# Performance work log

Measured on AMD Instinct MI355X. Metric: run time of the kernel, lower is better.

## Reference

```python
import jax, jax.numpy as jnp
import numpy as np

N, E, G = 50000, 150000, 200
D, ED_IN, EH = 320, 15, 32
NB, NT = 3, 9  # conv blocks, edge types


def setup_inputs() -> dict:
    key = jax.random.key(0)
    ks = jax.random.split(key, 16)
    s = 0.02
    return {
        "x": jax.random.normal(ks[0], (N, D), jnp.float32),
        "batch": jnp.sort(jax.random.randint(ks[1], (N,), 0, G)),
        "edge_indices": jax.random.randint(ks[2], (NT, 2, E), 0, N),
        "edge_attrs": jax.random.normal(ks[3], (NT, E, ED_IN), jnp.float32),
        "W1": jax.random.normal(ks[4], (2 * D + ED_IN, EH), jnp.float32) * s,
        "b1": jnp.zeros((EH,), jnp.float32),
        "W2": jax.random.normal(ks[5], (EH, EH), jnp.float32) * s,
        "b2": jnp.zeros((EH,), jnp.float32),
        "Wq": jax.random.normal(ks[6], (NB, NT, D, D), jnp.float32) * s,
        "bq": jnp.zeros((NB, NT, D), jnp.float32),
        "Wk": jax.random.normal(ks[7], (NB, NT, D, D), jnp.float32) * s,
        "bk": jnp.zeros((NB, NT, D), jnp.float32),
        "Wv": jax.random.normal(ks[8], (NB, NT, D, D), jnp.float32) * s,
        "bv": jnp.zeros((NB, NT, D), jnp.float32),
        "We": jax.random.normal(ks[9], (NB, NT, EH, D), jnp.float32) * s,
        "be": jnp.zeros((NB, NT, D), jnp.float32),
        "Ws": jax.random.normal(ks[10], (NB, NT, D, D), jnp.float32) * s,
        "bs": jnp.zeros((NB, NT, D), jnp.float32),
        "gamma": jnp.ones((NB, D), jnp.float32),
        "beta": jnp.zeros((NB, D), jnp.float32),
    }


def _transformer_conv(x, src, dst, ea, Wq, bq, Wk, bk, Wv, bv, We, be, Ws, bs):
    # PyG TransformerConv, heads=1, edge_dim=EH, eval mode (no dropout).
    q = (x @ Wq + bq)[dst]                    # [E, D] query at destination
    e = ea @ We + be                          # [E, D] projected edge attr
    k = (x @ Wk + bk)[src] + e                # [E, D]
    v = (x @ Wv + bv)[src] + e                # [E, D]
    alpha = (q * k).sum(-1) / jnp.sqrt(jnp.float32(D))  # [E]
    amax = jax.ops.segment_max(alpha, dst, num_segments=N)
    amax = jnp.where(jnp.isfinite(amax), amax, 0.0)     # guard empty segments
    ex = jnp.exp(alpha - amax[dst])
    denom = jax.ops.segment_sum(ex, dst, num_segments=N)
    w = ex / (denom[dst] + 1e-16)
    out = jax.ops.segment_sum(w[:, None] * v, dst, num_segments=N)
    return out + x @ Ws + bs                  # root/skip connection


def _graph_layer_norm(x, batch, gamma, beta):
    # PyG gnn.norm.LayerNorm, mode='graph': normalize per graph over nodes+channels.
    cnt = jax.ops.segment_sum(jnp.ones((N,), x.dtype), batch, num_segments=G)
    norm = jnp.maximum(cnt, 1.0) * D          # elements per graph
    mean = jax.ops.segment_sum(x.sum(-1), batch, num_segments=G) / norm
    xc = x - mean[batch][:, None]
    var = jax.ops.segment_sum((xc * xc).sum(-1), batch, num_segments=G) / norm
    out = xc / jnp.sqrt(var + 1e-5)[batch][:, None]
    return out * gamma + beta


def reference(x, batch, edge_indices, edge_attrs, W1, b1, W2, b2,
              Wq, bq, Wk, bk, Wv, bv, We, be, Ws, bs, gamma, beta):
    # Edge MLP preprocessing (uses original node features x).
    new_ea = []
    for t in range(NT):
        src, dst = edge_indices[t, 0], edge_indices[t, 1]
        cat = jnp.concatenate([x[src], x[dst], edge_attrs[t]], axis=-1)  # [E, 655]
        h = jax.nn.leaky_relu(cat @ W1 + b1)
        new_ea.append(h @ W2 + b2)

    h = x
    for b in range(NB):
        acc = jnp.zeros_like(h)
        for t in range(NT):
            src, dst = edge_indices[t, 0], edge_indices[t, 1]
            acc = acc + _transformer_conv(
                h, src, dst, new_ea[t],
                Wq[b, t], bq[b, t], Wk[b, t], bk[b, t], Wv[b, t], bv[b, t],
                We[b, t], be[b, t], Ws[b, t], bs[b, t])
        x_ = jax.nn.leaky_relu(acc / 9.0)
        x_ = _graph_layer_norm(x_, batch, gamma[b], beta[b])
        h = 0.5 * (h + x_)

    return jax.ops.segment_max(h, batch, num_segments=G)  # global max pool [G, D]
```

## Files before the change

kernel.cpp:

```cpp
#include <hip/hip_runtime.h>

#define N_NODES 50000
#define N_EDGE  150000
#define N_GRAPH 200
#define DIM     320
#define EDI     15
#define EH      32
#define NBLK    3
#define NTYP    9
#define NPAD    51200
#define BPT     50
#define QLD     676
#define QCOLS   673
#define NPQ     768

typedef unsigned short u16;
typedef unsigned int   u32;
typedef __bf16 bf16x8 __attribute__((ext_vector_type(8)));
typedef float  f32x4  __attribute__((ext_vector_type(4)));

__device__ __forceinline__ float b2f(u16 s) {
    u32 u = ((u32)s) << 16;
    return __builtin_bit_cast(float, u);
}
__device__ __forceinline__ float b2f_lo(u32 u) { return __builtin_bit_cast(float, u << 16); }
__device__ __forceinline__ float b2f_hi(u32 u) { return __builtin_bit_cast(float, u & 0xffff0000u); }
__device__ __forceinline__ u16 f2b(float f) {
    u32 u = __builtin_bit_cast(u32, f);
    u = (u + 0x7fffu + ((u >> 16) & 1u)) >> 16;
    return (u16)u;
}

__device__ __forceinline__ void gll16(const u16* g, u32 ldsAddr) {
    u32 m0v = (u32)__builtin_amdgcn_readfirstlane((int)ldsAddr);
    asm volatile("s_mov_b32 m0, %0\n\t"
                 "global_load_lds_dwordx4 %1, off"
                 :: "s"(m0v), "v"((unsigned long long)(size_t)g)
                 : "memory");
}

__global__ __launch_bounds__(256) void gemm_kernel(
    const u16* __restrict__ A, int Mstride,
    const u16* __restrict__ Bst, const float* __restrict__ bias,
    u16* __restrict__ Cb, float* __restrict__ Cf,
    int ldc, int out_cols, int M, int NP, int KQ, int mode)
{
    const int tid = threadIdx.x;
    const int wave = tid >> 6, lane = tid & 63;

    const int nwg = gridDim.x * gridDim.y;
    const int flat = blockIdx.y * gridDim.x + blockIdx.x;
    const int qq = nwg >> 3, rr = nwg & 7;
    const int xcd = flat & 7, loc = flat >> 3;
    const int swz = (xcd < rr ? xcd * (qq + 1) : rr * (qq + 1) + (xcd - rr) * qq) + loc;
    const int n0 = (swz % gridDim.x) * 128, m0 = (swz / gridDim.x) * 128;

    const int wm = (wave & 1) << 6, wn = (wave >> 1) << 6;
    const int lm = lane & 15, quad = lane >> 4;

    __shared__ uint4 smem[2][2][512];
    const u32 ldsBase = (u32)(size_t)&smem[0][0][0];

    f32x4 acc[4][4] = {};
    const int nIter = KQ >> 2;

    auto stage = [&](int s, int buf) {
        const int c0 = s << 2;
        const u32 bufBase = ldsBase + (u32)buf * 16384u;
#pragma unroll
        for (int u = 0; u < 2; ++u) {
            const int i = wave + (u << 2);
            const int chunk = i >> 1, half = (i & 1) << 6;
            const u16* ga = A + ((size_t)(c0 + chunk) * Mstride + m0 + half + lane) * 8;
            gll16(ga, bufBase + (u32)i * 1024u);
            const u16* gb = Bst + ((size_t)(c0 + chunk) * NP + n0 + half + lane) * 8;
            gll16(gb, bufBase + 8192u + (u32)i * 1024u);
        }
    };

    stage(0, 0);
    asm volatile("s_waitcnt vmcnt(0)" ::: "memory");
    __syncthreads();

    int cur = 0;
    for (int s = 0; s < nIter; ++s) {
        if (s + 1 < nIter) stage(s + 1, cur ^ 1);
        const uint4* aT = &smem[cur][0][0];
        const uint4* bT = &smem[cur][1][0];
        bf16x8 af[4], bfr[4];
#pragma unroll
        for (int mi = 0; mi < 4; ++mi)
            af[mi] = __builtin_bit_cast(bf16x8, aT[quad * 128 + wm + mi * 16 + lm]);
#pragma unroll
        for (int ni = 0; ni < 4; ++ni)
            bfr[ni] = __builtin_bit_cast(bf16x8, bT[quad * 128 + wn + ni * 16 + lm]);
#pragma unroll
        for (int mi = 0; mi < 4; ++mi)
#pragma unroll
            for (int ni = 0; ni < 4; ++ni)
                acc[mi][ni] = __builtin_amdgcn_mfma_f32_16x16x32_bf16(af[mi], bfr[ni], acc[mi][ni], 0, 0, 0);
        asm volatile("s_waitcnt vmcnt(0)" ::: "memory");
        __syncthreads();
        cur ^= 1;
    }

#pragma unroll
    for (int mi = 0; mi < 4; ++mi) {
        int row = m0 + wm + mi * 16 + quad * 4;
#pragma unroll
        for (int ni = 0; ni < 4; ++ni) {
            int col = n0 + wn + ni * 16 + lm;
            float bv = bias ? bias[col] : 0.f;
#pragma unroll
            for (int r = 0; r < 4; ++r) {
                int rr2 = row + r;
                if (rr2 < M && col < out_cols) {
                    float v = acc[mi][ni][r] + bv;
                    size_t off = (size_t)rr2 * ldc + col;
                    if (mode == 0)      Cb[off] = f2b(v);
                    else if (mode == 1) Cf[off] = v;
                    else                Cf[off] += v;
                }
            }
        }
    }
}

__global__ void k_convert_x(const float* __restrict__ x, u16* __restrict__ hb,
                            u16* __restrict__ hNode) {
    int i = blockIdx.x * 256 + threadIdx.x;
    if (i >= N_NODES * DIM) return;
    int node = i / DIM, c = i - node * DIM;
    u16 v = f2b(x[i]);
    hb[((size_t)(c >> 3) * N_NODES + node) * 8 + (c & 7)] = v;
    hNode[i] = v;
}

__global__ __launch_bounds__(256) void k_prep_M(
    const float* __restrict__ Wq, const float* __restrict__ Wk,
    float* __restrict__ Mf)
{
    __shared__ float aq[16][321];
    __shared__ float ak[16][321];
    int bt = blockIdx.z, e0 = blockIdx.y * 16, d0 = blockIdx.x * 16;
    const float* wq = Wq + ((size_t)bt * 320 + e0) * 320;
    const float* wk = Wk + ((size_t)bt * 320 + d0) * 320;
    for (int i = threadIdx.x; i < 16 * 320; i += 256) {
        int r = i / 320, j = i - r * 320;
        aq[r][j] = wq[(size_t)r * 320 + j];
        ak[r][j] = wk[(size_t)r * 320 + j];
    }
    __syncthreads();
    int te = threadIdx.x >> 4, td = threadIdx.x & 15;
    float s = 0.f;
    for (int j = 0; j < 320; ++j) s += aq[te][j] * ak[td][j];
    Mf[((size_t)bt * 320 + e0 + te) * 320 + d0 + td] = s;
}

__global__ void k_prep_qkvW(const float* __restrict__ Mf, const float* __restrict__ Wv,
                            u16* __restrict__ Bst) {
    int i = blockIdx.x * 256 + threadIdx.x;
    if (i >= 27 * 40 * NPQ) return;
    int col = i % NPQ, kq = (i / NPQ) % 40, bt = i / (NPQ * 40);
    if (col >= 640 && col < QCOLS) return;
    u16 tmp[8];
    if (col >= QCOLS) {
#pragma unroll
        for (int r = 0; r < 8; ++r) tmp[r] = 0;
    } else if (col < 320) {
#pragma unroll
        for (int r = 0; r < 8; ++r)
            tmp[r] = f2b(Mf[((size_t)bt * 320 + kq * 8 + r) * 320 + col]);
    } else {
#pragma unroll
        for (int r = 0; r < 8; ++r)
            tmp[r] = f2b(Wv[((size_t)bt * 320 + kq * 8 + r) * 320 + (col - 320)]);
    }
    *(uint4*)(&Bst[(((size_t)bt * 40 + kq) * NPQ + col) * 8]) = *(uint4*)tmp;
}

__global__ __launch_bounds__(256) void k_prep_ext(
    const float* __restrict__ Wq, const float* __restrict__ bq,
    const float* __restrict__ We, const float* __restrict__ be,
    const float* __restrict__ bk,
    u16* __restrict__ Bst, float* __restrict__ biasQkv)
{
    __shared__ float WeL[33 * 321];
    int bt = blockIdx.x, kt = blockIdx.y;
    for (int i = threadIdx.x; i < 33 * 320; i += 256) {
        int r = i / 320, d = i - r * 320;
        WeL[r * 321 + d] = (r < 32) ? We[((size_t)bt * 32 + r) * 320 + d]
                                    : (be[(size_t)bt * 320 + d] + bk[(size_t)bt * 320 + d]);
    }
    __syncthreads();
    if (kt < 10) {
        int k  = kt * 32 + (threadIdx.x >> 3);
        int ct = threadIdx.x & 7;
        const float* wq = Wq + ((size_t)bt * 320 + k) * 320;
        float dot[5] = {0.f, 0.f, 0.f, 0.f, 0.f};
        for (int d = 0; d < 320; ++d) {
            float w = wq[d];
            dot[0] += w * WeL[ct * 321 + d];
            dot[1] += w * WeL[(ct + 8) * 321 + d];
            dot[2] += w * WeL[(ct + 16) * 321 + d];
            dot[3] += w * WeL[(ct + 24) * 321 + d];
            dot[4] += w * WeL[32 * 321 + d];
        }
#pragma unroll
        for (int u = 0; u < 4; ++u)
            Bst[(((size_t)bt * 40 + (k >> 3)) * NPQ + 640 + ct + u * 8) * 8 + (k & 7)] = f2b(dot[u]);
        if (ct == 0)
            Bst[(((size_t)bt * 40 + (k >> 3)) * NPQ + 672) * 8 + (k & 7)] = f2b(dot[4]);
    } else {
        int c = threadIdx.x;
        if (c < 33) {
            const float* b = bq + (size_t)bt * 320;
            float s = 0.f;
            for (int d = 0; d < 320; ++d) s += b[d] * WeL[c * 321 + d];
            biasQkv[bt * 1024 + 640 + c] = s;
        }
    }
}

__global__ __launch_bounds__(256) void k_prep_qkvB(
    const float* __restrict__ Wk, const float* __restrict__ bq,
    const float* __restrict__ bv, float* __restrict__ bias)
{
    int i = blockIdx.x * 256 + threadIdx.x;
    if (i >= 27 * NPQ) return;
    int col = i % NPQ, bt = i / NPQ;
    if (col < 320) {
        const float4* wr = (const float4*)(Wk + ((size_t)bt * 320 + col) * 320);
        const float4* bb = (const float4*)(bq + (size_t)bt * 320);
        float s = 0.f;
        for (int j = 0; j < 80; ++j) {
            float4 a = wr[j], b = bb[j];
            s += a.x * b.x + a.y * b.y + a.z * b.z + a.w * b.w;
        }
        bias[bt * 1024 + col] = s;
    } else if (col < 640) {
        bias[bt * 1024 + col] = bv[(size_t)bt * 320 + (col - 320)];
    } else if (col >= QCOLS) {
        bias[bt * 1024 + col] = 0.f;
    }
}

__global__ void k_prep_skipW(const float* __restrict__ Ws, u16* __restrict__ Bst) {
    int i = blockIdx.x * 256 + threadIdx.x;
    if (i >= 3 * 320 * 384) return;
    int col = i % 384, k = (i / 384) % 320, b = i / (384 * 320);
    float v = 0.f;
    if (col < 320)
        for (int t = 0; t < 9; ++t)
            v += Ws[((size_t)(b * 9 + t) * 320 + k) * 320 + col];
    Bst[(((size_t)b * 40 + (k >> 3)) * 384 + col) * 8 + (k & 7)] = f2b(v);
}
__global__ void k_prep_skipB(const float* __restrict__ bs, float* __restrict__ bias) {
    int i = blockIdx.x * 256 + threadIdx.x;
    if (i >= 3 * 384) return;
    int col = i % 384, b = i / 384;
    float v = 0.f;
    if (col < 320)
        for (int t = 0; t < 9; ++t) v += bs[(b * 9 + t) * 320 + col];
    bias[i] = v;
}

__global__ void k_prep_sWe(const float* __restrict__ We, const float* __restrict__ be,
                           u16* __restrict__ Bst) {
    int i = blockIdx.x * 256 + threadIdx.x;
    if (i >= 3 * 40 * 384) return;
    int col = i % 384, kq = (i / 384) % 40, b = i / (384 * 40);
    u16 tmp[8];
#pragma unroll
    for (int r = 0; r < 8; ++r) {
        int k = kq * 8 + r;
        float v = 0.f;
        if (col < 320 && k < 306) {
            int t = k / 34, j = k - t * 34;
            int bt = b * 9 + t;
            if (j < 32)       v = We[((size_t)bt * 32 + j) * 320 + col];
            else if (j == 32) v = be[(size_t)bt * 320 + col];
        }
        tmp[r] = f2b(v);
    }
    *(uint4*)(&Bst[(((size_t)b * 40 + kq) * 384 + col) * 8]) = *(uint4*)tmp;
}

__global__ void k_prep_w1W(const float* __restrict__ W1, u16* __restrict__ Bst) {
    int i = blockIdx.x * 256 + threadIdx.x;
    if (i >= 320 * 128) return;
    int col = i & 127, k = i >> 7;
    float v = 0.f;
    if (col < 32)      v = W1[(size_t)k * 32 + col];
    else if (col < 64) v = W1[(size_t)(320 + k) * 32 + (col - 32)];
    Bst[((size_t)(k >> 3) * 128 + col) * 8 + (k & 7)] = f2b(v);
}

__global__ void k_csr_zero(int* __restrict__ cnt) {
    int i = blockIdx.x * 256 + threadIdx.x;
    if (i < NTYP * NPAD) cnt[i] = 0;
}
__global__ void k_csr_count(const int* __restrict__ eidx, int* __restrict__ cnt) {
    int i = blockIdx.x * 256 + threadIdx.x;
    if (i >= NTYP * N_EDGE) return;
    int t = i / N_EDGE, e = i - t * N_EDGE;
    int dst = eidx[(size_t)(t * 2 + 1) * N_EDGE + e];
    atomicAdd(&cnt[t * NPAD + dst], 1);
}
__global__ __launch_bounds__(1024) void k_csr_scan1(const int* __restrict__ cnt,
                                                    int* __restrict__ rowStart,
                                                    int* __restrict__ blockSum) {
    __shared__ int tmp[1024];
    int t = blockIdx.y, blk = blockIdx.x, tid = threadIdx.x;
    int idx = t * NPAD + blk * 1024 + tid;
    int v = cnt[idx];
    tmp[tid] = v;
    __syncthreads();
    for (int off = 1; off < 1024; off <<= 1) {
        int x = (tid >= off) ? tmp[tid - off] : 0;
        __syncthreads();
        tmp[tid] += x;
        __syncthreads();
    }
    rowStart[idx] = tmp[tid] - v;
    if (tid == 1023) blockSum[t * 64 + blk] = tmp[tid];
}
__global__ void k_csr_scan2(int* __restrict__ blockSum) {
    int t = threadIdx.x;
    if (t >= NTYP) return;
    int run = 0;
    for (int b = 0; b < BPT; ++b) {
        int v = blockSum[t * 64 + b];
        blockSum[t * 64 + b] = run;
        run += v;
    }
}
__global__ void k_csr_scan3(int* __restrict__ rowStart, const int* __restrict__ blockSum,
                            int* __restrict__ cursor) {
    int i = blockIdx.x * 256 + threadIdx.x;
    if (i >= NTYP * NPAD) return;
    int t = i / NPAD, n = i - t * NPAD;
    int v = rowStart[i] + blockSum[t * 64 + (n >> 10)];
    rowStart[i] = v;
    cursor[i] = v;
}
__global__ void k_csr_scatter(const int* __restrict__ eidx, int* __restrict__ cursor,
                              u16* __restrict__ sSrc, int* __restrict__ sEid) {
    int i = blockIdx.x * 256 + threadIdx.x;
    if (i >= NTYP * N_EDGE) return;
    int t = i / N_EDGE, e = i - t * N_EDGE;
    int src = eidx[(size_t)(t * 2) * N_EDGE + e];
    int dst = eidx[(size_t)(t * 2 + 1) * N_EDGE + e];
    int pos = atomicAdd(&cursor[t * NPAD + dst], 1);
    sSrc[(size_t)t * N_EDGE + pos] = (u16)src;
    sEid[(size_t)t * N_EDGE + pos] = e;
}

__global__ __launch_bounds__(256) void k_edge_mlp(
    const u16* __restrict__ Anodes, const int* __restrict__ eidx,
    const float* __restrict__ eattr, const float* __restrict__ W1,
    const float* __restrict__ b1, const float* __restrict__ W2,
    const float* __restrict__ b2, u16* __restrict__ outEa, int t)
{
    __shared__ float w1c[EDI][EH];
    __shared__ float w2s[EH][EH];
    __shared__ float b1s[EH], b2s[EH];
    int tid = threadIdx.x;
    for (int i = tid; i < EDI * EH; i += 256) w1c[i / EH][i % EH] = W1[(640 + i / EH) * EH + (i % EH)];
    for (int i = tid; i < EH * EH; i += 256) w2s[i / EH][i % EH] = W2[i];
    if (tid < EH) { b1s[tid] = b1[tid]; b2s[tid] = b2[tid]; }
    __syncthreads();

    int e = blockIdx.x * 256 + tid;
    if (e >= N_EDGE) return;
    int src = eidx[(size_t)(t * 2) * N_EDGE + e];
    int dst = eidx[(size_t)(t * 2 + 1) * N_EDGE + e];
    const float* eat = eattr + ((size_t)t * N_EDGE + e) * EDI;
    const u16* a1 = Anodes + (size_t)src * 64;
    const u16* a2 = Anodes + (size_t)dst * 64 + 32;

    float h1[EH];
#pragma unroll
    for (int j = 0; j < EH; ++j) h1[j] = b2f(a1[j]) + b2f(a2[j]) + b1s[j];
    for (int i = 0; i < EDI; ++i) {
        float v = eat[i];
#pragma unroll
        for (int j = 0; j < EH; ++j) h1[j] += v * w1c[i][j];
    }
#pragma unroll
    for (int j = 0; j < EH; ++j) h1[j] = h1[j] > 0.f ? h1[j] : 0.01f * h1[j];

    u16* orow = outEa + (size_t)e * EH;
    for (int j = 0; j < EH; ++j) {
        float o = b2s[j];
#pragma unroll
        for (int i = 0; i < EH; ++i) o += h1[i] * w2s[i][j];
        orow[j] = f2b(o);
    }
}

__global__ __launch_bounds__(256) void k_attn(
    const u16* __restrict__ qkv, const u16* __restrict__ hNode,
    const int* __restrict__ rowStart,
    const u16* __restrict__ sSrc, const int* __restrict__ sEid,
    const u16* __restrict__ ea, float* __restrict__ acc,
    u16* __restrict__ sST, int t34)
{
    int wave = threadIdx.x >> 6, lane = threadIdx.x & 63;
    int n = blockIdx.x * 4 + wave;
    if (n >= N_NODES) return;
    int eb = rowStart[n], ee = rowStart[n + 1];
    if (eb == ee) return;

    const u16* qrow = qkv + (size_t)n * QLD;
    uint2 qv = *(const uint2*)(qrow + 4 * lane);
    float q40 = b2f_lo(qv.x), q41 = b2f_hi(qv.x);
    float q42 = b2f_lo(qv.y), q43 = b2f_hi(qv.y);
    float q1 = b2f(qrow[256 + lane]);
    float qwl = (lane < 33) ? b2f(qrow[640 + lane]) : 0.f;
    float qwbe = __shfl(qwl, 32, 64);
    float qw = (lane < 32) ? qwl : 0.f;
    const float RS = 0.05590169943749474f;

    float m = -INFINITY, l = 0.f, as = 0.f;
    float av0 = 0.f, av1 = 0.f, av2 = 0.f, av3 = 0.f, avt = 0.f;

    int ei = eb;
    for (; ei + 2 <= ee; ei += 2) {
        int s0 = sSrc[ei], s1 = sSrc[ei + 1];
        int id0 = sEid[ei], id1 = sEid[ei + 1];
        const u16* kr0 = hNode + (size_t)s0 * DIM;
        const u16* kr1 = hNode + (size_t)s1 * DIM;
        uint2 k0v = *(const uint2*)(kr0 + 4 * lane);
        uint2 k1v = *(const uint2*)(kr1 + 4 * lane);
        float k0t = b2f(kr0[256 + lane]);
        float k1t = b2f(kr1[256 + lane]);
        float ea0 = (lane < 32) ? b2f(ea[(size_t)id0 * 32 + lane]) : 0.f;
        float ea1 = (lane < 32) ? b2f(ea[(size_t)id1 * 32 + lane]) : 0.f;
        float d0 = qw * ea0 + q1 * k0t
                 + q40 * b2f_lo(k0v.x) + q41 * b2f_hi(k0v.x)
                 + q42 * b2f_lo(k0v.y) + q43 * b2f_hi(k0v.y);
        float d1 = qw * ea1 + q1 * k1t
                 + q40 * b2f_lo(k1v.x) + q41 * b2f_hi(k1v.x)
                 + q42 * b2f_lo(k1v.y) + q43 * b2f_hi(k1v.y);
#pragma unroll
        for (int off = 32; off > 0; off >>= 1) {
            d0 += __shfl_xor(d0, off, 64);
            d1 += __shfl_xor(d1, off, 64);
        }
        float a0 = (d0 + qwbe) * RS, a1 = (d1 + qwbe) * RS;
        float mn = fmaxf(m, fmaxf(a0, a1));
        float sc = __expf(m - mn);
        float p0 = __expf(a0 - mn), p1 = __expf(a1 - mn);
        l = l * sc + p0 + p1;
        const u16* vr0 = qkv + (size_t)s0 * QLD + 320;
        const u16* vr1 = qkv + (size_t)s1 * QLD + 320;
        uint2 v0v = *(const uint2*)(vr0 + 4 * lane);
        uint2 v1v = *(const uint2*)(vr1 + 4 * lane);
        float v0t = b2f(vr0[256 + lane]), v1t = b2f(vr1[256 + lane]);
        av0 = av0 * sc + p0 * b2f_lo(v0v.x) + p1 * b2f_lo(v1v.x);
        av1 = av1 * sc + p0 * b2f_hi(v0v.x) + p1 * b2f_hi(v1v.x);
        av2 = av2 * sc + p0 * b2f_lo(v0v.y) + p1 * b2f_lo(v1v.y);
        av3 = av3 * sc + p0 * b2f_hi(v0v.y) + p1 * b2f_hi(v1v.y);
        avt = avt * sc + p0 * v0t + p1 * v1t;
        as = as * sc + p0 * ea0 + p1 * ea1;
        m = mn;
    }
    if (ei < ee) {
        int s0 = sSrc[ei];
        int id0 = sEid[ei];
        const u16* kr0 = hNode + (size_t)s0 * DIM;
        uint2 k0v = *(const uint2*)(kr0 + 4 * lane);
        float k0t = b2f(kr0[256 + lane]);
        float ea0 = (lane < 32) ? b2f(ea[(size_t)id0 * 32 + lane]) : 0.f;
        float d0 = qw * ea0 + q1 * k0t
                 + q40 * b2f_lo(k0v.x) + q41 * b2f_hi(k0v.x)
                 + q42 * b2f_lo(k0v.y) + q43 * b2f_hi(k0v.y);
#pragma unroll
        for (int off = 32; off > 0; off >>= 1) d0 += __shfl_xor(d0, off, 64);
        float a0 = (d0 + qwbe) * RS;
        float mn = fmaxf(m, a0);
        float sc = __expf(m - mn), p0 = __expf(a0 - mn);
        l = l * sc + p0;
        const u16* vr0 = qkv + (size_t)s0 * QLD + 320;
        uint2 v0v = *(const uint2*)(vr0 + 4 * lane);
        float v0t = b2f(vr0[256 + lane]);
        av0 = av0 * sc + p0 * b2f_lo(v0v.x);
        av1 = av1 * sc + p0 * b2f_hi(v0v.x);
        av2 = av2 * sc + p0 * b2f_lo(v0v.y);
        av3 = av3 * sc + p0 * b2f_hi(v0v.y);
        avt = avt * sc + p0 * v0t;
        as = as * sc + p0 * ea0;
    }

    float inv = 1.f / l;
    float* arow = acc + (size_t)n * DIM;
    f32x4 pa = *(const f32x4*)(arow + 4 * lane);
    pa[0] += av0 * inv; pa[1] += av1 * inv;
    pa[2] += av2 * inv; pa[3] += av3 * inv;
    *(f32x4*)(arow + 4 * lane) = pa;
    arow[256 + lane] += avt * inv;
    if (lane < 33) {
        int k = t34 + lane;
        float sv = (lane < 32) ? as * inv : 1.f;
        sST[((size_t)(k >> 3) * N_NODES + n) * 8 + (k & 7)] = f2b(sv);
    }
}

__device__ __forceinline__ int lowerb(const int* a, int n, int v) {
    int lo = 0, hi = n;
    while (lo < hi) { int mid = (lo + hi) >> 1; if (a[mid] < v) lo = mid + 1; else hi = mid; }
    return lo;
}

__global__ __launch_bounds__(1024) void k_post(
    const float* __restrict__ acc, u16* __restrict__ hb, u16* __restrict__ hNode,
    const int* __restrict__ batch, const float* __restrict__ gamma,
    const float* __restrict__ beta)
{
    int g = blockIdx.x;
    int start = lowerb(batch, N_NODES, g);
    int end   = lowerb(batch, N_NODES, g + 1);
    int cnt = end - start;
    if (cnt == 0) return;
    int i0 = start * DIM, i1 = end * DIM;

    float s = 0.f, ss = 0.f;
    for (int i = i0 + threadIdx.x; i < i1; i += 1024) {
        float v = acc[i] * (1.f / 9.f);
        v = v > 0.f ? v : 0.01f * v;
        s += v; ss += v * v;
    }
    __shared__ float rs[16], rss[16];
#pragma unroll
    for (int off = 32; off > 0; off >>= 1) { s += __shfl_xor(s, off, 64); ss += __shfl_xor(ss, off, 64); }
    int wave = threadIdx.x >> 6, lane = threadIdx.x & 63;
    if (lane == 0) { rs[wave] = s; rss[wave] = ss; }
    __syncthreads();
    if (threadIdx.x == 0) {
        float S = 0.f, SS = 0.f;
        for (int w = 0; w < 16; ++w) { S += rs[w]; SS += rss[w]; }
        float norm = (float)cnt * DIM;
        float mean = S / norm;
        float var = SS / norm - mean * mean;
        rs[0] = mean;
        rss[0] = rsqrtf(var + 1e-5f);
    }
    __syncthreads();
    float mean = rs[0], rsig = rss[0];
    for (int i = i0 + threadIdx.x; i < i1; i += 1024) {
        float v = acc[i] * (1.f / 9.f);
        v = v > 0.f ? v : 0.01f * v;
        int node = i / DIM, c = i - node * DIM;
        float o = (v - mean) * rsig * gamma[c] + beta[c];
        u16 nb = f2b(0.5f * (b2f(hNode[i]) + o));
        hNode[i] = nb;
        hb[((size_t)(c >> 3) * N_NODES + node) * 8 + (c & 7)] = nb;
    }
}

__global__ __launch_bounds__(320) void k_maxpool(
    const u16* __restrict__ hb, const int* __restrict__ batch, float* __restrict__ out)
{
    int g = blockIdx.x, c = threadIdx.x;
    int start = lowerb(batch, N_NODES, g);
    int end   = lowerb(batch, N_NODES, g + 1);
    size_t base = (size_t)(c >> 3) * N_NODES * 8 + (c & 7);
    float m = -INFINITY;
    for (int n = start; n < end; ++n) m = fmaxf(m, b2f(hb[base + (size_t)n * 8]));
    out[(size_t)g * DIM + c] = m;
}

extern "C" void kernel_launch(void* const* d_in, const int* in_sizes, int n_in,
                              void* d_out, int out_size, void* d_ws, size_t ws_size,
                              hipStream_t stream)
{
    (void)in_sizes; (void)n_in; (void)out_size;
    const float* x     = (const float*)d_in[0];
    const int*   batch = (const int*)d_in[1];
    const int*   eidx  = (const int*)d_in[2];
    const float* eattr = (const float*)d_in[3];
    const float* W1 = (const float*)d_in[4];
    const float* b1 = (const float*)d_in[5];
    const float* W2 = (const float*)d_in[6];
    const float* b2 = (const float*)d_in[7];
    const float* Wq = (const float*)d_in[8];
    const float* bq = (const float*)d_in[9];
    const float* Wk = (const float*)d_in[10];
    const float* bk = (const float*)d_in[11];
    const float* Wv = (const float*)d_in[12];
    const float* bv = (const float*)d_in[13];
    const float* We = (const float*)d_in[14];
    const float* be = (const float*)d_in[15];
    const float* Ws = (const float*)d_in[16];
    const float* bs = (const float*)d_in[17];
    const float* gamma = (const float*)d_in[18];
    const float* beta  = (const float*)d_in[19];
    float* out = (float*)d_out;

    char* base = (char*)d_ws;
    size_t off = 0;
    auto carve = [&](size_t bytes) -> char* {
        char* r = base + off;
        off += (bytes + 255) & ~(size_t)255;
        return r;
    };
    u16*   hbKq    = (u16*)  carve((size_t)40 * N_NODES * 8 * 2 + 1024);
    u16*   hNode   = (u16*)  carve((size_t)N_NODES * DIM * 2);
    float* acc     = (float*)carve((size_t)N_NODES * DIM * 4);
    u16*   qkv     = (u16*)  carve((size_t)N_NODES * QLD * 2);
    u16*   sST     = (u16*)  carve((size_t)40 * N_NODES * 8 * 2 + 1024);
    u16*   Anodes  = (u16*)  carve((size_t)N_NODES * 64 * 2);
    float* Mf      = (float*)carve((size_t)27 * 320 * 320 * 4);
    u16*   BstQkv  = (u16*)  carve((size_t)27 * 40 * NPQ * 8 * 2);
    float* biasQkv = (float*)carve((size_t)27 * 1024 * 4);
    u16*   BstSkip = (u16*)  carve((size_t)3 * 40 * 384 * 8 * 2);
    float* biasSkip= (float*)carve((size_t)3 * 384 * 4);
    u16*   BstSWe  = (u16*)  carve((size_t)3 * 40 * 384 * 8 * 2);
    u16*   BstW1   = (u16*)  carve((size_t)40 * 128 * 8 * 2);
    int*   cnt     = (int*)  carve((size_t)NTYP * NPAD * 4);
    int*   rowStart= (int*)  carve((size_t)NTYP * NPAD * 4);
    int*   blockSum= (int*)  carve((size_t)NTYP * 64 * 4);
    u16*   sSrc    = (u16*)  carve((size_t)NTYP * N_EDGE * 2);
    int*   sEid    = (int*)  carve((size_t)NTYP * N_EDGE * 4);
    size_t fixed = off;
    size_t bigBytes   = (size_t)NTYP * N_EDGE * EH * 2;
    size_t smallBytes = (size_t)N_EDGE * EH * 2;
    int bigEa = (ws_size >= fixed + bigBytes + (1u << 20)) ? 1 : 0;
    u16* newEa = (u16*)carve(bigEa ? bigBytes : smallBytes);

    k_convert_x<<<(N_NODES * DIM + 255) / 256, 256, 0, stream>>>(x, hbKq, hNode);
    k_prep_M<<<dim3(20, 20, 27), 256, 0, stream>>>(Wq, Wk, Mf);
    k_prep_qkvW<<<(27 * 40 * NPQ + 255) / 256, 256, 0, stream>>>(Mf, Wv, BstQkv);
    k_prep_ext<<<dim3(27, 11), 256, 0, stream>>>(Wq, bq, We, be, bk, BstQkv, biasQkv);
    k_prep_qkvB<<<(27 * NPQ + 255) / 256, 256, 0, stream>>>(Wk, bq, bv, biasQkv);
    k_prep_skipW<<<(3 * 320 * 384 + 255) / 256, 256, 0, stream>>>(Ws, BstSkip);
    k_prep_skipB<<<(3 * 384 + 255) / 256, 256, 0, stream>>>(bs, biasSkip);
    k_prep_sWe<<<(3 * 40 * 384 + 255) / 256, 256, 0, stream>>>(We, be, BstSWe);
    k_prep_w1W<<<(320 * 128 + 255) / 256, 256, 0, stream>>>(W1, BstW1);

    k_csr_zero<<<(NTYP * NPAD + 255) / 256, 256, 0, stream>>>(cnt);
    k_csr_count<<<(NTYP * N_EDGE + 255) / 256, 256, 0, stream>>>(eidx, cnt);
    k_csr_scan1<<<dim3(BPT, NTYP), 1024, 0, stream>>>(cnt, rowStart, blockSum);
    k_csr_scan2<<<1, 64, 0, stream>>>(blockSum);
    k_csr_scan3<<<(NTYP * NPAD + 255) / 256, 256, 0, stream>>>(rowStart, blockSum, cnt);
    k_csr_scatter<<<(NTYP * N_EDGE + 255) / 256, 256, 0, stream>>>(eidx, cnt, sSrc, sEid);

    const int mt = (N_NODES + 127) / 128;
    const int et = (N_EDGE + 255) / 256;
    gemm_kernel<<<dim3(1, mt), 256, 0, stream>>>(hbKq, N_NODES, BstW1, nullptr,
                                                 Anodes, nullptr, 64, 64, N_NODES, 128, 40, 0);
    if (bigEa) {
        for (int t = 0; t < NTYP; ++t)
            k_edge_mlp<<<dim3(et), 256, 0, stream>>>(
                Anodes, eidx, eattr, W1, b1, W2, b2, newEa + (size_t)t * N_EDGE * EH, t);
    }

    for (int b = 0; b < NBLK; ++b) {
        gemm_kernel<<<dim3(3, mt), 256, 0, stream>>>(
            hbKq, N_NODES, BstSkip + (size_t)b * 40 * 384 * 8, biasSkip + b * 384,
            nullptr, acc, DIM, DIM, N_NODES, 384, 40, 1);
        hipMemsetAsync(sST, 0, (size_t)40 * N_NODES * 8 * 2, stream);
        for (int t = 0; t < NTYP; ++t) {
            int bt = b * NTYP + t;
            u16* eaT = bigEa ? (newEa + (size_t)t * N_EDGE * EH) : newEa;
            if (!bigEa)
                k_edge_mlp<<<dim3(et), 256, 0, stream>>>(
                    Anodes, eidx, eattr, W1, b1, W2, b2, eaT, t);
            gemm_kernel<<<dim3(6, mt), 256, 0, stream>>>(
                hbKq, N_NODES, BstQkv + (size_t)bt * 40 * NPQ * 8, biasQkv + bt * 1024,
                qkv, nullptr, QLD, QCOLS, N_NODES, NPQ, 40, 0);
            k_attn<<<dim3((N_NODES + 3) / 4), 256, 0, stream>>>(
                qkv, hNode, rowStart + t * NPAD, sSrc + (size_t)t * N_EDGE, sEid + (size_t)t * N_EDGE,
                eaT, acc, sST, t * 34);
        }
        gemm_kernel<<<dim3(3, mt), 256, 0, stream>>>(
            sST, N_NODES, BstSWe + (size_t)b * 40 * 384 * 8, nullptr,
            nullptr, acc, DIM, DIM, N_NODES, 384, 40, 2);
        k_post<<<N_GRAPH, 1024, 0, stream>>>(acc, hbKq, hNode, batch,
                                             gamma + b * DIM, beta + b * DIM);
    }
    k_maxpool<<<N_GRAPH, 320, 0, stream>>>(hbKq, batch, out);
}
```

Measured before the change: 5.768 ms.

## Defer V projection: aggregate raw source features, apply Wv in batched GEMMs

The per-type QKV GEMM no longer computes the V columns, which halves its output width. The attention kernel instead aggregates the softmax-weighted raw source node features and edge attributes into a bf16 K-major staging buffer. Wv, We, the biases and the skip weights are then applied through grouped GEMMs with larger K that accumulate into acc every two edge types. The Wq·Wk^T precompute also moves onto the MFMA GEMM with a batched z dimension. This trades per-type V GEMM work for fewer, deeper GEMMs and lighter attention writes, but adds bf16 rounding of the aggregated features and a more complex buffer-reuse layout.

After: 5.523 ms. 1.04x faster.

```diff
diff --git a/kernel.cpp b/kernel.cpp
--- a/kernel.cpp
+++ b/kernel.cpp
@@ -10,9 +10,11 @@
 #define NTYP    9
 #define NPAD    51200
 #define BPT     50
-#define QLD     676
-#define QCOLS   673
-#define NPQ     768
+#define QLD     360
+#define QCOLS   353
+#define NPQ     384
+#define HAGCH   132
+#define BIGCH   448
 
 typedef unsigned short u16;
 typedef unsigned int   u32;
@@ -43,8 +45,14 @@
     const u16* __restrict__ A, int Mstride,
     const u16* __restrict__ Bst, const float* __restrict__ bias,
     u16* __restrict__ Cb, float* __restrict__ Cf,
-    int ldc, int out_cols, int M, int NP, int KQ, int mode)
-{
+    int ldc, int out_cols, int M, int NP, int KQ, int mode,
+    int zA, int zB, int zC)
+{
+    A += (size_t)blockIdx.z * zA;
+    Bst += (size_t)blockIdx.z * zB;
+    if (Cb) Cb += (size_t)blockIdx.z * zC;
+    if (Cf) Cf += (size_t)blockIdx.z * zC;
+
     const int tid = threadIdx.x;
     const int wave = tid >> 6, lane = tid & 63;
 
@@ -136,45 +144,30 @@
     hNode[i] = v;
 }
 
-__global__ __launch_bounds__(256) void k_prep_M(
-    const float* __restrict__ Wq, const float* __restrict__ Wk,
-    float* __restrict__ Mf)
-{
-    __shared__ float aq[16][321];
-    __shared__ float ak[16][321];
-    int bt = blockIdx.z, e0 = blockIdx.y * 16, d0 = blockIdx.x * 16;
-    const float* wq = Wq + ((size_t)bt * 320 + e0) * 320;
-    const float* wk = Wk + ((size_t)bt * 320 + d0) * 320;
-    for (int i = threadIdx.x; i < 16 * 320; i += 256) {
-        int r = i / 320, j = i - r * 320;
-        aq[r][j] = wq[(size_t)r * 320 + j];
-        ak[r][j] = wk[(size_t)r * 320 + j];
-    }
-    __syncthreads();
-    int te = threadIdx.x >> 4, td = threadIdx.x & 15;
-    float s = 0.f;
-    for (int j = 0; j < 320; ++j) s += aq[te][j] * ak[td][j];
-    Mf[((size_t)bt * 320 + e0 + te) * 320 + d0 + td] = s;
-}
-
-__global__ void k_prep_qkvW(const float* __restrict__ Mf, const float* __restrict__ Wv,
-                            u16* __restrict__ Bst) {
+__global__ void k_prep_wT(const float* __restrict__ W, u16* __restrict__ T) {
+    int i = blockIdx.x * 256 + threadIdx.x;
+    if (i >= 27 * 40 * 320) return;
+    int e = i % 320, jq = (i / 320) % 40, bt = i / (320 * 40);
+    const float* src = W + ((size_t)bt * 320 + e) * 320 + jq * 8;
+    u16 tmp[8];
+#pragma unroll
+    for (int r = 0; r < 8; ++r) tmp[r] = f2b(src[r]);
+    *(uint4*)(&T[(((size_t)bt * 40 + jq) * 320 + e) * 8]) = *(uint4*)tmp;
+}
+
+__global__ void k_prep_qkvW(const u16* __restrict__ Mb, u16* __restrict__ Bst) {
     int i = blockIdx.x * 256 + threadIdx.x;
     if (i >= 27 * 40 * NPQ) return;
     int col = i % NPQ, kq = (i / NPQ) % 40, bt = i / (NPQ * 40);
-    if (col >= 640 && col < QCOLS) return;
+    if (col >= 320 && col < QCOLS) return;
     u16 tmp[8];
     if (col >= QCOLS) {
 #pragma unroll
         for (int r = 0; r < 8; ++r) tmp[r] = 0;
-    } else if (col < 320) {
+    } else {
 #pragma unroll
         for (int r = 0; r < 8; ++r)
-            tmp[r] = f2b(Mf[((size_t)bt * 320 + kq * 8 + r) * 320 + col]);
-    } else {
-#pragma unroll
-        for (int r = 0; r < 8; ++r)
-            tmp[r] = f2b(Wv[((size_t)bt * 320 + kq * 8 + r) * 320 + (col - 320)]);
+            tmp[r] = Mb[((size_t)bt * 320 + kq * 8 + r) * 320 + col];
     }
     *(uint4*)(&Bst[(((size_t)bt * 40 + kq) * NPQ + col) * 8]) = *(uint4*)tmp;
 }
@@ -208,23 +201,23 @@
         }
 #pragma unroll
         for (int u = 0; u < 4; ++u)
-            Bst[(((size_t)bt * 40 + (k >> 3)) * NPQ + 640 + ct + u * 8) * 8 + (k & 7)] = f2b(dot[u]);
+            Bst[(((size_t)bt * 40 + (k >> 3)) * NPQ + 320 + ct + u * 8) * 8 + (k & 7)] = f2b(dot[u]);
         if (ct == 0)
-            Bst[(((size_t)bt * 40 + (k >> 3)) * NPQ + 672) * 8 + (k & 7)] = f2b(dot[4]);
+            Bst[(((size_t)bt * 40 + (k >> 3)) * NPQ + 352) * 8 + (k & 7)] = f2b(dot[4]);
     } else {
         int c = threadIdx.x;
         if (c < 33) {
             const float* b = bq + (size_t)bt * 320;
             float s = 0.f;
             for (int d = 0; d < 320; ++d) s += b[d] * WeL[c * 321 + d];
-            biasQkv[bt * 1024 + 640 + c] = s;
+            biasQkv[bt * NPQ + 320 + c] = s;
         }
     }
 }
 
 __global__ __launch_bounds__(256) void k_prep_qkvB(
     const float* __restrict__ Wk, const float* __restrict__ bq,
-    const float* __restrict__ bv, float* __restrict__ bias)
+    float* __restrict__ bias)
 {
     int i = blockIdx.x * 256 + threadIdx.x;
     if (i >= 27 * NPQ) return;
@@ -237,24 +230,12 @@
             float4 a = wr[j], b = bb[j];
             s += a.x * b.x + a.y * b.y + a.z * b.z + a.w * b.w;
         }
-        bias[bt * 1024 + col] = s;
-    } else if (col < 640) {
-        bias[bt * 1024 + col] = bv[(size_t)bt * 320 + (col - 320)];
+        bias[bt * NPQ + col] = s;
     } else if (col >= QCOLS) {
-        bias[bt * 1024 + col] = 0.f;
-    }
-}
-
-__global__ void k_prep_skipW(const float* __restrict__ Ws, u16* __restrict__ Bst) {
-    int i = blockIdx.x * 256 + threadIdx.x;
-    if (i >= 3 * 320 * 384) return;
-    int col = i % 384, k = (i / 384) % 320, b = i / (384 * 320);
-    float v = 0.f;
-    if (col < 320)
-        for (int t = 0; t < 9; ++t)
-            v += Ws[((size_t)(b * 9 + t) * 320 + k) * 320 + col];
-    Bst[(((size_t)b * 40 + (k >> 3)) * 384 + col) * 8 + (k & 7)] = f2b(v);
-}
+        bias[bt * NPQ + col] = 0.f;
+    }
+}
+
 __global__ void k_prep_skipB(const float* __restrict__ bs, float* __restrict__ bias) {
     int i = blockIdx.x * 256 + threadIdx.x;
     if (i >= 3 * 384) return;
@@ -265,25 +246,34 @@
     bias[i] = v;
 }
 
-__global__ void k_prep_sWe(const float* __restrict__ We, const float* __restrict__ be,
-                           u16* __restrict__ Bst) {
-    int i = blockIdx.x * 256 + threadIdx.x;
-    if (i >= 3 * 40 * 384) return;
-    int col = i % 384, kq = (i / 384) % 40, b = i / (384 * 40);
+__global__ void k_prep_bigB(const float* __restrict__ Ws, const float* __restrict__ Wv,
+                            const float* __restrict__ We, const float* __restrict__ be,
+                            const float* __restrict__ bv, u16* __restrict__ Bst) {
+    int i = blockIdx.x * 256 + threadIdx.x;
+    if (i >= 3 * BIGCH * 384) return;
+    int col = i % 384, q = (i / 384) % BIGCH, b = i / (384 * BIGCH);
     u16 tmp[8];
 #pragma unroll
     for (int r = 0; r < 8; ++r) {
-        int k = kq * 8 + r;
+        int k = q * 8 + r;
         float v = 0.f;
-        if (col < 320 && k < 306) {
-            int t = k / 34, j = k - t * 34;
-            int bt = b * 9 + t;
-            if (j < 32)       v = We[((size_t)bt * 32 + j) * 320 + col];
-            else if (j == 32) v = be[(size_t)bt * 320 + col];
+        if (col < 320) {
+            if (k < 320) {
+                for (int t = 0; t < 9; ++t)
+                    v += Ws[((size_t)(b * 9 + t) * 320 + k) * 320 + col];
+            } else {
+                int kk = k - 320, t = kk / 360, kl = kk - t * 360;
+                if (t < 9) {
+                    int bt = b * 9 + t;
+                    if (kl < 320)       v = Wv[((size_t)bt * 320 + kl) * 320 + col];
+                    else if (kl < 352)  v = We[((size_t)bt * 32 + (kl - 320)) * 320 + col];
+                    else if (kl == 352) v = be[(size_t)bt * 320 + col] + bv[(size_t)bt * 320 + col];
+                }
+            }
         }
         tmp[r] = f2b(v);
     }
-    *(uint4*)(&Bst[(((size_t)b * 40 + kq) * 384 + col) * 8]) = *(uint4*)tmp;
+    *(uint4*)(&Bst[(((size_t)b * BIGCH + q) * 384 + col) * 8]) = *(uint4*)tmp;
 }
 
 __global__ void k_prep_w1W(const float* __restrict__ W1, u16* __restrict__ Bst) {
@@ -403,107 +393,100 @@
     const u16* __restrict__ qkv, const u16* __restrict__ hNode,
     const int* __restrict__ rowStart,
     const u16* __restrict__ sSrc, const int* __restrict__ sEid,
-    const u16* __restrict__ ea, float* __restrict__ acc,
-    u16* __restrict__ sST, int t34)
+    const u16* __restrict__ ea, u16* __restrict__ hA, int cb)
 {
     int wave = threadIdx.x >> 6, lane = threadIdx.x & 63;
     int n = blockIdx.x * 4 + wave;
     if (n >= N_NODES) return;
     int eb = rowStart[n], ee = rowStart[n + 1];
-    if (eb == ee) return;
-
-    const u16* qrow = qkv + (size_t)n * QLD;
-    uint2 qv = *(const uint2*)(qrow + 4 * lane);
-    float q40 = b2f_lo(qv.x), q41 = b2f_hi(qv.x);
-    float q42 = b2f_lo(qv.y), q43 = b2f_hi(qv.y);
-    float q1 = b2f(qrow[256 + lane]);
-    float qwl = (lane < 33) ? b2f(qrow[640 + lane]) : 0.f;
-    float qwbe = __shfl(qwl, 32, 64);
-    float qw = (lane < 32) ? qwl : 0.f;
-    const float RS = 0.05590169943749474f;
-
-    float m = -INFINITY, l = 0.f, as = 0.f;
+
+    float l = 0.f, as = 0.f;
     float av0 = 0.f, av1 = 0.f, av2 = 0.f, av3 = 0.f, avt = 0.f;
 
-    int ei = eb;
-    for (; ei + 2 <= ee; ei += 2) {
-        int s0 = sSrc[ei], s1 = sSrc[ei + 1];
-        int id0 = sEid[ei], id1 = sEid[ei + 1];
-        const u16* kr0 = hNode + (size_t)s0 * DIM;
-        const u16* kr1 = hNode + (size_t)s1 * DIM;
-        uint2 k0v = *(const uint2*)(kr0 + 4 * lane);
-        uint2 k1v = *(const uint2*)(kr1 + 4 * lane);
-        float k0t = b2f(kr0[256 + lane]);
-        float k1t = b2f(kr1[256 + lane]);
-        float ea0 = (lane < 32) ? b2f(ea[(size_t)id0 * 32 + lane]) : 0.f;
-        float ea1 = (lane < 32) ? b2f(ea[(size_t)id1 * 32 + lane]) : 0.f;
-        float d0 = qw * ea0 + q1 * k0t
-                 + q40 * b2f_lo(k0v.x) + q41 * b2f_hi(k0v.x)
-                 + q42 * b2f_lo(k0v.y) + q43 * b2f_hi(k0v.y);
-        float d1 = qw * ea1 + q1 * k1t
-                 + q40 * b2f_lo(k1v.x) + q41 * b2f_hi(k1v.x)
-                 + q42 * b2f_lo(k1v.y) + q43 * b2f_hi(k1v.y);
-#pragma unroll
-        for (int off = 32; off > 0; off >>= 1) {
-            d0 += __shfl_xor(d0, off, 64);
-            d1 += __shfl_xor(d1, off, 64);
-        }
-        float a0 = (d0 + qwbe) * RS, a1 = (d1 + qwbe) * RS;
-        float mn = fmaxf(m, fmaxf(a0, a1));
-        float sc = __expf(m - mn);
-        float p0 = __expf(a0 - mn), p1 = __expf(a1 - mn);
-        l = l * sc + p0 + p1;
-        const u16* vr0 = qkv + (size_t)s0 * QLD + 320;
-        const u16* vr1 = qkv + (size_t)s1 * QLD + 320;
-        uint2 v0v = *(const uint2*)(vr0 + 4 * lane);
-        uint2 v1v = *(const uint2*)(vr1 + 4 * lane);
-        float v0t = b2f(vr0[256 + lane]), v1t = b2f(vr1[256 + lane]);
-        av0 = av0 * sc + p0 * b2f_lo(v0v.x) + p1 * b2f_lo(v1v.x);
-        av1 = av1 * sc + p0 * b2f_hi(v0v.x) + p1 * b2f_hi(v1v.x);
-        av2 = av2 * sc + p0 * b2f_lo(v0v.y) + p1 * b2f_lo(v1v.y);
-        av3 = av3 * sc + p0 * b2f_hi(v0v.y) + p1 * b2f_hi(v1v.y);
-        avt = avt * sc + p0 * v0t + p1 * v1t;
-        as = as * sc + p0 * ea0 + p1 * ea1;
-        m = mn;
-    }
-    if (ei < ee) {
-        int s0 = sSrc[ei];
-        int id0 = sEid[ei];
-        const u16* kr0 = hNode + (size_t)s0 * DIM;
-        uint2 k0v = *(const uint2*)(kr0 + 4 * lane);
-        float k0t = b2f(kr0[256 + lane]);
-        float ea0 = (lane < 32) ? b2f(ea[(size_t)id0 * 32 + lane]) : 0.f;
-        float d0 = qw * ea0 + q1 * k0t
-                 + q40 * b2f_lo(k0v.x) + q41 * b2f_hi(k0v.x)
-                 + q42 * b2f_lo(k0v.y) + q43 * b2f_hi(k0v.y);
-#pragma unroll
-        for (int off = 32; off > 0; off >>= 1) d0 += __shfl_xor(d0, off, 64);
-        float a0 = (d0 + qwbe) * RS;
-        float mn = fmaxf(m, a0);
-        float sc = __expf(m - mn), p0 = __expf(a0 - mn);
-        l = l * sc + p0;
-        const u16* vr0 = qkv + (size_t)s0 * QLD + 320;
-        uint2 v0v = *(const uint2*)(vr0 + 4 * lane);
-        float v0t = b2f(vr0[256 + lane]);
-        av0 = av0 * sc + p0 * b2f_lo(v0v.x);
-        av1 = av1 * sc + p0 * b2f_hi(v0v.x);
-        av2 = av2 * sc + p0 * b2f_lo(v0v.y);
-        av3 = av3 * sc + p0 * b2f_hi(v0v.y);
-        avt = avt * sc + p0 * v0t;
-        as = as * sc + p0 * ea0;
-    }
-
-    float inv = 1.f / l;
-    float* arow = acc + (size_t)n * DIM;
-    f32x4 pa = *(const f32x4*)(arow + 4 * lane);
-    pa[0] += av0 * inv; pa[1] += av1 * inv;
-    pa[2] += av2 * inv; pa[3] += av3 * inv;
-    *(f32x4*)(arow + 4 * lane) = pa;
-    arow[256 + lane] += avt * inv;
-    if (lane < 33) {
-        int k = t34 + lane;
-        float sv = (lane < 32) ? as * inv : 1.f;
-        sST[((size_t)(k >> 3) * N_NODES + n) * 8 + (k & 7)] = f2b(sv);
+    if (eb != ee) {
+        const u16* qrow = qkv + (size_t)n * QLD;
+        uint2 qv = *(const uint2*)(qrow + 4 * lane);
+        float q40 = b2f_lo(qv.x), q41 = b2f_hi(qv.x);
+        float q42 = b2f_lo(qv.y), q43 = b2f_hi(qv.y);
+        float q1 = b2f(qrow[256 + lane]);
+        float qwl = (lane < 33) ? b2f(qrow[320 + lane]) : 0.f;
+        float qwbe = __shfl(qwl, 32, 64);
+        float qw = (lane < 32) ? qwl : 0.f;
+        const float RS = 0.05590169943749474f;
+        float m = -INFINITY;
+
+        int ei = eb;
+        for (; ei + 2 <= ee; ei += 2) {
+            int s0 = sSrc[ei], s1 = sSrc[ei + 1];
+            int id0 = sEid[ei], id1 = sEid[ei + 1];
+            const u16* kr0 = hNode + (size_t)s0 * DIM;
+            const u16* kr1 = hNode + (size_t)s1 * DIM;
+            uint2 k0v = *(const uint2*)(kr0 + 4 * lane);
+            uint2 k1v = *(const uint2*)(kr1 + 4 * lane);
+            float k00 = b2f_lo(k0v.x), k01 = b2f_hi(k0v.x);
+            float k02 = b2f_lo(k0v.y), k03 = b2f_hi(k0v.y);
+            float k10 = b2f_lo(k1v.x), k11 = b2f_hi(k1v.x);
+            float k12 = b2f_lo(k1v.y), k13 = b2f_hi(k1v.y);
+            float k0t = b2f(kr0[256 + lane]);
+            float k1t = b2f(kr1[256 + lane]);
+            float ea0 = (lane < 32) ? b2f(ea[(size_t)id0 * 32 + lane]) : 0.f;
+            float ea1 = (lane < 32) ? b2f(ea[(size_t)id1 * 32 + lane]) : 0.f;
+            float d0 = qw * ea0 + q1 * k0t + q40 * k00 + q41 * k01 + q42 * k02 + q43 * k03;
+            float d1 = qw * ea1 + q1 * k1t + q40 * k10 + q41 * k11 + q42 * k12 + q43 * k13;
+#pragma unroll
+            for (int off = 32; off > 0; off >>= 1) {
+                d0 += __shfl_xor(d0, off, 64);
+                d1 += __shfl_xor(d1, off, 64);
+            }
+            float a0 = (d0 + qwbe) * RS, a1 = (d1 + qwbe) * RS;
+            float mn = fmaxf(m, fmaxf(a0, a1));
+            float sc = __expf(m - mn);
+            float p0 = __expf(a0 - mn), p1 = __expf(a1 - mn);
+            l = l * sc + p0 + p1;
+            av0 = av0 * sc + p0 * k00 + p1 * k10;
+            av1 = av1 * sc + p0 * k01 + p1 * k11;
+            av2 = av2 * sc + p0 * k02 + p1 * k12;
+            av3 = av3 * sc + p0 * k03 + p1 * k13;
+            avt = avt * sc + p0 * k0t + p1 * k1t;
+            as = as * sc + p0 * ea0 + p1 * ea1;
+            m = mn;
+        }
+        if (ei < ee) {
+            int s0 = sSrc[ei];
+            int id0 = sEid[ei];
+            const u16* kr0 = hNode + (size_t)s0 * DIM;
+            uint2 k0v = *(const uint2*)(kr0 + 4 * lane);
+            float k00 = b2f_lo(k0v.x), k01 = b2f_hi(k0v.x);
+            float k02 = b2f_lo(k0v.y), k03 = b2f_hi(k0v.y);
+            float k0t = b2f(kr0[256 + lane]);
+            float ea0 = (lane < 32) ? b2f(ea[(size_t)id0 * 32 + lane]) : 0.f;
+            float d0 = qw * ea0 + q1 * k0t + q40 * k00 + q41 * k01 + q42 * k02 + q43 * k03;
+#pragma unroll
+            for (int off = 32; off > 0; off >>= 1) d0 += __shfl_xor(d0, off, 64);
+            float a0 = (d0 + qwbe) * RS;
+            float mn = fmaxf(m, a0);
+            float sc = __expf(m - mn), p0 = __expf(a0 - mn);
+            l = l * sc + p0;
+            av0 = av0 * sc + p0 * k00;
+            av1 = av1 * sc + p0 * k01;
+            av2 = av2 * sc + p0 * k02;
+            av3 = av3 * sc + p0 * k03;
+            avt = avt * sc + p0 * k0t;
+            as = as * sc + p0 * ea0;
+        }
+    }
+
+    float inv = (l > 0.f) ? 1.f / l : 0.f;
+    u32 w0 = (u32)f2b(av0 * inv) | ((u32)f2b(av1 * inv) << 16);
+    u32 w1 = (u32)f2b(av2 * inv) | ((u32)f2b(av3 * inv) << 16);
+    uint2 wv; wv.x = w0; wv.y = w1;
+    *(uint2*)(hA + ((size_t)(cb + (lane >> 1)) * N_NODES + n) * 8 + (lane & 1) * 4) = wv;
+    hA[((size_t)(cb + 32 + (lane >> 3)) * N_NODES + n) * 8 + (lane & 7)] = f2b(avt * inv);
+    if (lane < 32) {
+        hA[((size_t)(cb + 40 + (lane >> 3)) * N_NODES + n) * 8 + (lane & 7)] = f2b(as * inv);
+    } else if (lane == 32) {
+        uint4 fz; fz.x = (eb != ee) ? 0x3f80u : 0u; fz.y = 0u; fz.z = 0u; fz.w = 0u;
+        *(uint4*)(hA + ((size_t)(cb + 44) * N_NODES + n) * 8) = fz;
     }
 }
 
@@ -605,18 +588,15 @@
         off += (bytes + 255) & ~(size_t)255;
         return r;
     };
-    u16*   hbKq    = (u16*)  carve((size_t)40 * N_NODES * 8 * 2 + 1024);
+    u16*   hAg     = (u16*)  carve((size_t)HAGCH * N_NODES * 8 * 2 + 1024);
     u16*   hNode   = (u16*)  carve((size_t)N_NODES * DIM * 2);
     float* acc     = (float*)carve((size_t)N_NODES * DIM * 4);
     u16*   qkv     = (u16*)  carve((size_t)N_NODES * QLD * 2);
-    u16*   sST     = (u16*)  carve((size_t)40 * N_NODES * 8 * 2 + 1024);
     u16*   Anodes  = (u16*)  carve((size_t)N_NODES * 64 * 2);
-    float* Mf      = (float*)carve((size_t)27 * 320 * 320 * 4);
     u16*   BstQkv  = (u16*)  carve((size_t)27 * 40 * NPQ * 8 * 2);
-    float* biasQkv = (float*)carve((size_t)27 * 1024 * 4);
-    u16*   BstSkip = (u16*)  carve((size_t)3 * 40 * 384 * 8 * 2);
+    float* biasQkv = (float*)carve((size_t)27 * NPQ * 4);
+    u16*   BstBig  = (u16*)  carve((size_t)3 * BIGCH * 384 * 8 * 2);
     float* biasSkip= (float*)carve((size_t)3 * 384 * 4);
-    u16*   BstSWe  = (u16*)  carve((size_t)3 * 40 * 384 * 8 * 2);
     u16*   BstW1   = (u16*)  carve((size_t)40 * 128 * 8 * 2);
     int*   cnt     = (int*)  carve((size_t)NTYP * NPAD * 4);
     int*   rowStart= (int*)  carve((size_t)NTYP * NPAD * 4);
@@ -629,14 +609,22 @@
     int bigEa = (ws_size >= fixed + bigBytes + (1u << 20)) ? 1 : 0;
     u16* newEa = (u16*)carve(bigEa ? bigBytes : smallBytes);
 
-    k_convert_x<<<(N_NODES * DIM + 255) / 256, 256, 0, stream>>>(x, hbKq, hNode);
-    k_prep_M<<<dim3(20, 20, 27), 256, 0, stream>>>(Wq, Wk, Mf);
-    k_prep_qkvW<<<(27 * 40 * NPQ + 255) / 256, 256, 0, stream>>>(Mf, Wv, BstQkv);
+    u16* regionB = hAg + (size_t)40 * N_NODES * 8;
+    u16* AqT = regionB;
+    u16* BkT = AqT + 27 * 40 * 320 * 8 + 512;
+    u16* Mb  = BkT + 27 * 40 * 320 * 8 + 512;
+
+    k_convert_x<<<(N_NODES * DIM + 255) / 256, 256, 0, stream>>>(x, hAg, hNode);
+    hipMemsetAsync(hAg + (size_t)130 * N_NODES * 8, 0, (size_t)2 * N_NODES * 8 * 2, stream);
+    k_prep_wT<<<(27 * 40 * 320 + 255) / 256, 256, 0, stream>>>(Wq, AqT);
+    k_prep_wT<<<(27 * 40 * 320 + 255) / 256, 256, 0, stream>>>(Wk, BkT);
+    gemm_kernel<<<dim3(3, 3, 27), 256, 0, stream>>>(AqT, 320, BkT, nullptr,
+        Mb, nullptr, 320, 320, 320, 320, 40, 0, 102400, 102400, 102400);
+    k_prep_qkvW<<<(27 * 40 * NPQ + 255) / 256, 256, 0, stream>>>(Mb, BstQkv);
     k_prep_ext<<<dim3(27, 11), 256, 0, stream>>>(Wq, bq, We, be, bk, BstQkv, biasQkv);
-    k_prep_qkvB<<<(27 * NPQ + 255) / 256, 256, 0, stream>>>(Wk, bq, bv, biasQkv);
-    k_prep_skipW<<<(3 * 320 * 384 + 255) / 256, 256, 0, stream>>>(Ws, BstSkip);
+    k_prep_qkvB<<<(27 * NPQ + 255) / 256, 256, 0, stream>>>(Wk, bq, biasQkv);
     k_prep_skipB<<<(3 * 384 + 255) / 256, 256, 0, stream>>>(bs, biasSkip);
-    k_prep_sWe<<<(3 * 40 * 384 + 255) / 256, 256, 0, stream>>>(We, be, BstSWe);
+    k_prep_bigB<<<(3 * BIGCH * 384 + 255) / 256, 256, 0, stream>>>(Ws, Wv, We, be, bv, BstBig);
     k_prep_w1W<<<(320 * 128 + 255) / 256, 256, 0, stream>>>(W1, BstW1);
 
     k_csr_zero<<<(NTYP * NPAD + 255) / 256, 256, 0, stream>>>(cnt);
@@ -648,37 +636,45 @@
 
     const int mt = (N_NODES + 127) / 128;
     const int et = (N_EDGE + 255) / 256;
-    gemm_kernel<<<dim3(1, mt), 256, 0, stream>>>(hbKq, N_NODES, BstW1, nullptr,
-                                                 Anodes, nullptr, 64, 64, N_NODES, 128, 40, 0);
+    gemm_kernel<<<dim3(1, mt), 256, 0, stream>>>(hAg, N_NODES, BstW1, nullptr,
+        Anodes, nullptr, 64, 64, N_NODES, 128, 40, 0, 0, 0, 0);
     if (bigEa) {
         for (int t = 0; t < NTYP; ++t)
             k_edge_mlp<<<dim3(et), 256, 0, stream>>>(
                 Anodes, eidx, eattr, W1, b1, W2, b2, newEa + (size_t)t * N_EDGE * EH, t);
     }
 
+    const int gOff[5] = {0, 130, 220, 310, 400};
+    const int gKQ[5]  = {132, 92, 92, 92, 48};
+
     for (int b = 0; b < NBLK; ++b) {
-        gemm_kernel<<<dim3(3, mt), 256, 0, stream>>>(
-            hbKq, N_NODES, BstSkip + (size_t)b * 40 * 384 * 8, biasSkip + b * 384,
-            nullptr, acc, DIM, DIM, N_NODES, 384, 40, 1);
-        hipMemsetAsync(sST, 0, (size_t)40 * N_NODES * 8 * 2, stream);
         for (int t = 0; t < NTYP; ++t) {
             int bt = b * NTYP + t;
             u16* eaT = bigEa ? (newEa + (size_t)t * N_EDGE * EH) : newEa;
             if (!bigEa)
                 k_edge_mlp<<<dim3(et), 256, 0, stream>>>(
                     Anodes, eidx, eattr, W1, b1, W2, b2, eaT, t);
-            gemm_kernel<<<dim3(6, mt), 256, 0, stream>>>(
-                hbKq, N_NODES, BstQkv + (size_t)bt * 40 * NPQ * 8, biasQkv + bt * 1024,
-                qkv, nullptr, QLD, QCOLS, N_NODES, NPQ, 40, 0);
-            k_attn<<<dim3((N_NODES + 3) / 4), 256, 0, stream>>>(
-                qkv, hNode, rowStart + t * NPAD, sSrc + (size_t)t * N_EDGE, sEid + (size_t)t * N_EDGE,
-                eaT, acc, sST, t * 34);
+            gemm_kernel<<<dim3(3, mt), 256, 0, stream>>>(
+                hAg, N_NODES, BstQkv + (size_t)bt * 40 * NPQ * 8, biasQkv + bt * NPQ,
+                qkv, nullptr, QLD, QCOLS, N_NODES, NPQ, 40, 0, 0, 0, 0);
+            k_attn<<<dim3(N_NODES / 4), 256, 0, stream>>>(
+                qkv, hNode, rowStart + t * NPAD, sSrc + (size_t)t * N_EDGE,
+                sEid + (size_t)t * N_EDGE, eaT, hAg, 40 + (t & 1) * 45);
+            if (t & 1) {
+                int g = t >> 1;
+                gemm_kernel<<<dim3(3, mt), 256, 0, stream>>>(
+                    (g == 0) ? hAg : regionB, N_NODES,
+                    BstBig + ((size_t)b * BIGCH + gOff[g]) * 384 * 8,
+                    (g == 0) ? (biasSkip + b * 384) : nullptr,
+                    nullptr, acc, DIM, DIM, N_NODES, 384, gKQ[g],
+                    (g == 0) ? 1 : 2, 0, 0, 0);
+            }
         }
         gemm_kernel<<<dim3(3, mt), 256, 0, stream>>>(
-            sST, N_NODES, BstSWe + (size_t)b * 40 * 384 * 8, nullptr,
-            nullptr, acc, DIM, DIM, N_NODES, 384, 40, 2);
-        k_post<<<N_GRAPH, 1024, 0, stream>>>(acc, hbKq, hNode, batch,
+            regionB, N_NODES, BstBig + ((size_t)b * BIGCH + gOff[4]) * 384 * 8, nullptr,
+            nullptr, acc, DIM, DIM, N_NODES, 384, gKQ[4], 2, 0, 0, 0);
+        k_post<<<N_GRAPH, 1024, 0, stream>>>(acc, hAg, hNode, batch,
                                              gamma + b * DIM, beta + b * DIM);
     }
-    k_maxpool<<<N_GRAPH, 320, 0, stream>>>(hbKq, batch, out);
-}
+    k_maxpool<<<N_GRAPH, 320, 0, stream>>>(hAg, batch, out);
+}
```
